# Kernel tuning notes

Measured on AMD Instinct MI355X. Metric: run time of the kernel, lower is better.

Reference implementation:

```python
import jax, jax.numpy as jnp
import numpy as np

B, N_QUBITS, N_LAYERS = 128, 14, 4


def _rx(theta):
    c = jnp.cos(theta / 2).astype(jnp.complex64)
    s = (-1j) * jnp.sin(theta / 2).astype(jnp.complex64)
    return jnp.stack([jnp.stack([c, s], -1), jnp.stack([s, c], -1)], -2)


def _ry(theta):
    c = jnp.cos(theta / 2)
    s = jnp.sin(theta / 2)
    return jnp.stack([jnp.stack([c, -s], -1), jnp.stack([s, c], -1)], -2).astype(jnp.complex64)


def _rz(theta):
    p = jnp.exp((-0.5j) * theta.astype(jnp.complex64))
    q = jnp.exp((0.5j) * theta.astype(jnp.complex64))
    z = jnp.zeros_like(p)
    return jnp.stack([jnp.stack([p, z], -1), jnp.stack([z, q], -1)], -2)


def _apply_1q(state, U, wire):
    # state: (B, 2, 2, ..., 2); U: (2,2) shared or (B,2,2) per-sample
    s = jnp.moveaxis(state, wire + 1, 1)
    if U.ndim == 2:
        s = jnp.einsum('ij,bj...->bi...', U, s)
    else:
        s = jnp.einsum('bij,bj...->bi...', U, s)
    return jnp.moveaxis(s, 1, wire + 1)


def _cnot(state, c, t):
    s = jnp.moveaxis(state, (c + 1, t + 1), (1, 2))  # (B, 2c, 2t, rest)
    s = jnp.concatenate([s[:, :1], s[:, 1:, ::-1]], axis=1)  # flip target where control=1
    return jnp.moveaxis(s, (1, 2), (c + 1, t + 1))


def _layer(state, rx_l, ry_l, rz_l, ent_l, n):
    for i in range(n):
        state = _apply_1q(state, _rx(rx_l[i]), i)
        state = _apply_1q(state, _ry(ry_l[i]), i)
        state = _apply_1q(state, _rz(rz_l[i]), i)
    for i in range(n - 1):
        state = _cnot(state, i, i + 1)
        state = _apply_1q(state, _rz(ent_l[i]), i + 1)
    return state


def _circuit(x, rx_p, ry_p, rz_p, ent_p):
    b, n = x.shape
    n_layers = rx_p.shape[0]
    scaled = jnp.tanh(x) * np.pi  # angle encoding, matches torch.tanh(x)*pi
    state = jnp.zeros((b,) + (2,) * n, jnp.complex64)
    state = state.at[(slice(None),) + (0,) * n].set(1.0)  # |0...0> per sample
    for i in range(n):  # per-sample RY encoding
        state = _apply_1q(state, _ry(scaled[:, i]), i)
    for l in range(n_layers):
        state = _layer(state, rx_p[l], ry_p[l], rz_p[l], ent_p[l], n)
    probs = state.real ** 2 + state.imag ** 2  # (B, 2, ..., 2) real
    outs = []
    for i in range(n):  # <Z_i> = P(bit_i=0) - P(bit_i=1)
        p = jnp.moveaxis(probs, i + 1, 1).reshape(b, 2, -1).sum(-1)
        outs.append(p[:, 0] - p[:, 1])
    return jnp.stack(outs, -1)  # (B, n_qubits)


def setup_inputs() -> dict:
    key = jax.random.key(0)
    k1, k2, k3, k4, k5 = jax.random.split(key, 5)
    return {
        'x': jax.random.normal(k1, (B, N_QUBITS), jnp.float32),
        'params_rx': jax.random.normal(k2, (N_LAYERS, N_QUBITS), jnp.float32),
        'params_ry': jax.random.normal(k3, (N_LAYERS, N_QUBITS), jnp.float32),
        'params_rz': jax.random.normal(k4, (N_LAYERS, N_QUBITS), jnp.float32),
        'params_entangle': jax.random.normal(k5, (N_LAYERS, N_QUBITS - 1), jnp.float32),
    }


def reference(x, params_rx, params_ry, params_rz, params_entangle):
    return _circuit(x, params_rx, params_ry, params_rz, params_entangle)
```

## Files before the change

kernel.cpp:

```cpp
#include <hip/hip_runtime.h>
#include <math.h>

#define NQ 14
#define NL 4
#define NS (1 << NQ)
#define NT 1024
#define APT (NS / NT)

struct c32 { float x, y; };
__device__ __forceinline__ c32 cmul(c32 a, c32 b) { return {a.x*b.x - a.y*b.y, a.x*b.y + a.y*b.x}; }
__device__ __forceinline__ c32 cadd(c32 a, c32 b) { return {a.x + b.x, a.y + b.y}; }

__device__ __forceinline__ c32 phase_mul(float2 p1, float2 p2, float2 f) {
    c32 ph = { p1.x*p2.x - p1.y*p2.y, p1.x*p2.y + p1.y*p2.x };
    return { ph.x*f.x - ph.y*f.y, ph.x*f.y + ph.y*f.x };
}

__device__ __forceinline__ void gate8(c32* v, const float* U, const int s) {
    float4 u0 = *(const float4*)U;
    float4 u1 = *(const float4*)(U + 4);
    c32 a00={u0.x,u0.y}, a01={u0.z,u0.w}, a10={u1.x,u1.y}, a11={u1.z,u1.w};
    #pragma unroll
    for (int k = 0; k < 8; ++k) {
        if (k & s) continue;
        c32 A = v[k], B = v[k | s];
        v[k]     = cadd(cmul(a00, A), cmul(a01, B));
        v[k | s] = cadd(cmul(a10, A), cmul(a11, B));
    }
}

__device__ __forceinline__ void gate4(c32* v, const float* U, const int s) {
    float4 u0 = *(const float4*)U;
    float4 u1 = *(const float4*)(U + 4);
    c32 a00={u0.x,u0.y}, a01={u0.z,u0.w}, a10={u1.x,u1.y}, a11={u1.z,u1.w};
    #pragma unroll
    for (int k = 0; k < 4; ++k) {
        if (k & s) continue;
        c32 A = v[k], B = v[k | s];
        v[k]     = cadd(cmul(a00, A), cmul(a01, B));
        v[k | s] = cadd(cmul(a10, A), cmul(a11, B));
    }
}

__device__ __forceinline__ void gate8sw(c32* v, const float* U, const int s, const int sw) {
    float4 u0 = *(const float4*)U;
    float4 u1 = *(const float4*)(U + 4);
    c32 n00={u0.x,u0.y}, n01={u0.z,u0.w}, n10={u1.x,u1.y}, n11={u1.z,u1.w};
    c32 a00 = sw ? n11 : n00;
    c32 a01 = sw ? n10 : n01;
    c32 a10 = sw ? n01 : n10;
    c32 a11 = sw ? n00 : n11;
    #pragma unroll
    for (int k = 0; k < 8; ++k) {
        if (k & s) continue;
        c32 A = v[k], B = v[k | s];
        v[k]     = cadd(cmul(a00, A), cmul(a01, B));
        v[k | s] = cadd(cmul(a10, A), cmul(a11, B));
    }
}

__global__ __launch_bounds__(NT) __attribute__((amdgpu_waves_per_eu(4, 4)))
void qc_kernel(const float* __restrict__ x,
               const float* __restrict__ prx,
               const float* __restrict__ pry,
               const float* __restrict__ prz,
               const float* __restrict__ pent,
               float* __restrict__ out)
{
    __shared__ float2 st[NS];
    __shared__ float  Um[NL][NQ][8];
    __shared__ float2 tloc[NL][128];
    __shared__ float2 thic[NL][64];
    __shared__ float  encc[NQ], encs[NQ];
    __shared__ float  red[NT/64][NQ];

    const int tid = threadIdx.x;
    const int b   = blockIdx.x;

    if (tid < NL*NQ) {
        int l = tid / NQ, q = tid % NQ;
        float hx = 0.5f*prx[l*NQ+q], hy = 0.5f*pry[l*NQ+q], hz = 0.5f*prz[l*NQ+q];
        float cx = cosf(hx), sx = sinf(hx);
        float cy = cosf(hy), sy = sinf(hy);
        float cz = cosf(hz), sz = sinf(hz);
        c32 m00 = { cy*cx,  sy*sx };
        c32 m01 = {-sy*cx, -cy*sx };
        c32 m10 = { sy*cx, -cy*sx };
        c32 m11 = { cy*cx, -sy*sx };
        c32 e0 = {cz, -sz}, e1 = {cz, sz};
        c32 u00 = cmul(e0, m00), u01 = cmul(e0, m01);
        c32 u10 = cmul(e1, m10), u11 = cmul(e1, m11);
        float* U = Um[l][q];
        U[0]=u00.x; U[1]=u00.y; U[2]=u01.x; U[3]=u01.y;
        U[4]=u10.x; U[5]=u10.y; U[6]=u11.x; U[7]=u11.y;
    } else if (tid >= 64 && tid < 64 + NL*192) {
        int t2 = tid - 64;
        int l = t2 / 192, r = t2 % 192;
        if (r < 128) {
            float a = 0.f;
            for (int p = 0; p < 7; ++p) {
                float th = 0.5f * pent[l*(NQ-1) + (12 - p)];
                a += ((r >> p) & 1) ? th : -th;
            }
            tloc[l][r] = make_float2(cosf(a), sinf(a));
        } else {
            int m = r - 128;
            float a = 0.f;
            for (int p = 0; p < 6; ++p) {
                float th = 0.5f * pent[l*(NQ-1) + (5 - p)];
                a += ((m >> p) & 1) ? th : -th;
            }
            thic[l][m] = make_float2(cosf(a), sinf(a));
        }
    } else if (tid >= 960 && tid < 960 + NQ) {
        int i = tid - 960;
        float th = tanhf(x[b*NQ + i]) * 3.14159265358979323846f;
        encc[i] = cosf(0.5f*th);
        encs[i] = sinf(0.5f*th);
    }
    __syncthreads();

    {
        float prodT = 1.f;
        #pragma unroll
        for (int p = 0; p < 10; ++p)
            prodT *= ((tid >> p) & 1) ? encs[13-p] : encc[13-p];
        #pragma unroll 1
        for (int h = 0; h < 2; ++h) {
            float ah = prodT * (h ? encs[0] : encc[0]);
            c32 v[8];
            #pragma unroll
            for (int m = 0; m < 8; ++m) {
                float a = ah
                        * ((m & 4) ? encs[1] : encc[1])
                        * ((m & 2) ? encs[2] : encc[2])
                        * ((m & 1) ? encs[3] : encc[3]);
                v[m] = { a, 0.f };
            }
            gate8(v, Um[0][1], 4);
            gate8(v, Um[0][2], 2);
            gate8(v, Um[0][3], 1);
            const int yb = (h << 13) | tid;
            #pragma unroll
            for (int m = 0; m < 8; ++m) st[yb + (m << 10)] = make_float2(v[m].x, v[m].y);
        }
    }
    __syncthreads();

    #pragma unroll 1
    for (int l = 0; l < NL; ++l) {
        if (l > 0) {
            #pragma unroll 1
            for (int h = 0; h < 2; ++h) {
                const int yb = (h << 13) | tid;
                c32 v[8];
                #pragma unroll
                for (int m = 0; m < 8; ++m) {
                    int y = yb + (m << 10);
                    int a = y ^ (y >> 1);
                    float2 f = st[a];
                    v[m] = phase_mul(tloc[l-1][y & 127], thic[l-1][(y >> 7) & 63], f);
                }
                gate8(v, Um[l][1], 4);
                gate8(v, Um[l][2], 2);
                gate8(v, Um[l][3], 1);
                __syncthreads();
                #pragma unroll
                for (int m = 0; m < 8; ++m) st[yb + (m << 10)] = make_float2(v[m].x, v[m].y);
            }
            __syncthreads();
        }

        #pragma unroll 1
        for (int m = 0; m < 2; ++m) {
            const int T  = tid + (m << 10);
            const int ib = ((T >> 8) << 10) | (T & 255);
            c32 v[8];
            #pragma unroll
            for (int k = 0; k < 8; ++k) {
                int a = ib + ((k & 4) ? 8192 : 0) + ((k & 2) ? 512 : 0) + ((k & 1) ? 256 : 0);
                float2 f = st[a];
                v[k] = {f.x, f.y};
            }
            gate8(v, Um[l][0], 4);
            gate8(v, Um[l][4], 2);
            gate8(v, Um[l][5], 1);
            #pragma unroll
            for (int k = 0; k < 8; ++k) {
                int a = ib + ((k & 4) ? 8192 : 0) + ((k & 2) ? 512 : 0) + ((k & 1) ? 256 : 0);
                st[a] = make_float2(v[k].x, v[k].y);
            }
        }
        __syncthreads();

        #pragma unroll 1
        for (int m = 0; m < 2; ++m) {
            const int T  = tid + (m << 10);
            const int ib = ((T >> 5) << 8) | (T & 31);
            c32 v[8];
            #pragma unroll
            for (int k = 0; k < 8; ++k) { float2 f = st[ib + (k << 5)]; v[k] = {f.x, f.y}; }
            gate8(v, Um[l][6], 4);
            gate8(v, Um[l][7], 2);
            gate8(v, Um[l][8], 1);
            #pragma unroll
            for (int k = 0; k < 8; ++k) st[ib + (k << 5)] = make_float2(v[k].x, v[k].y);
        }
        __syncthreads();

        #pragma unroll 1
        for (int m = 0; m < 4; ++m) {
            const int T  = tid + (m << 10);
            const int ib = ((T >> 3) << 5) | (T & 7);
            c32 v[4];
            #pragma unroll
            for (int k = 0; k < 4; ++k) { float2 f = st[ib + (k << 3)]; v[k] = {f.x, f.y}; }
            gate4(v, Um[l][9], 2);
            gate4(v, Um[l][10], 1);
            #pragma unroll
            for (int k = 0; k < 4; ++k) st[ib + (k << 3)] = make_float2(v[k].x, v[k].y);
        }
        __syncthreads();

        {
            const int t4   = tid & 15;
            const int base = tid << 4;
            #pragma unroll 1
            for (int m = 0; m < 2; ++m) {
                c32 v[8];
                #pragma unroll
                for (int s = 0; s < 8; ++s) {
                    float2 f = st[base | (((m << 3) | s) ^ t4)];
                    v[s] = {f.x, f.y};
                }
                gate8sw(v, Um[l][11], 4, (t4 >> 2) & 1);
                gate8sw(v, Um[l][12], 2, (t4 >> 1) & 1);
                gate8sw(v, Um[l][13], 1,  t4       & 1);
                #pragma unroll
                for (int s = 0; s < 8; ++s)
                    st[base | (((m << 3) | s) ^ t4)] = make_float2(v[s].x, v[s].y);
            }
        }
        __syncthreads();
    }

    float acc[NQ];
    #pragma unroll
    for (int i = 0; i < NQ; ++i) acc[i] = 0.f;
    #pragma unroll
    for (int j = 0; j < APT; ++j) {
        int y = tid + j*NT;
        int a = y ^ (y >> 1);
        float2 f = st[a];
        c32 r = phase_mul(tloc[NL-1][y & 127], thic[NL-1][(y >> 7) & 63], f);
        float pr = r.x*r.x + r.y*r.y;
        #pragma unroll
        for (int p = 0; p < NQ; ++p)
            acc[NQ-1-p] += ((y >> p) & 1) ? -pr : pr;
    }
    #pragma unroll
    for (int off = 32; off >= 1; off >>= 1) {
        #pragma unroll
        for (int i = 0; i < NQ; ++i)
            acc[i] += __shfl_down(acc[i], off, 64);
    }
    const int wid = tid >> 6, lane = tid & 63;
    if (lane == 0) {
        #pragma unroll
        for (int i = 0; i < NQ; ++i) red[wid][i] = acc[i];
    }
    __syncthreads();
    if (tid < NQ) {
        float s = 0.f;
        #pragma unroll
        for (int w = 0; w < NT/64; ++w) s += red[w][tid];
        out[b*NQ + tid] = s;
    }
}

extern "C" void kernel_launch(void* const* d_in, const int* in_sizes, int n_in,
                              void* d_out, int out_size, void* d_ws, size_t ws_size,
                              hipStream_t stream) {
    (void)d_ws; (void)ws_size; (void)n_in; (void)out_size;
    const float* x    = (const float*)d_in[0];
    const float* prx  = (const float*)d_in[1];
    const float* pry  = (const float*)d_in[2];
    const float* prz  = (const float*)d_in[3];
    const float* pent = (const float*)d_in[4];
    float* out = (float*)d_out;
    const int B = in_sizes[0] / NQ;
    qc_kernel<<<B, NT, 0, stream>>>(x, prx, pry, prz, pent, out);
}
```

Before: 132.6 us.

## Regroup low-qubit gate passes per wavefront to drop block barriers

```diff
diff --git a/kernel.cpp b/kernel.cpp
--- a/kernel.cpp
+++ b/kernel.cpp
@@ -22,19 +22,6 @@
     c32 a00={u0.x,u0.y}, a01={u0.z,u0.w}, a10={u1.x,u1.y}, a11={u1.z,u1.w};
     #pragma unroll
     for (int k = 0; k < 8; ++k) {
-        if (k & s) continue;
-        c32 A = v[k], B = v[k | s];
-        v[k]     = cadd(cmul(a00, A), cmul(a01, B));
-        v[k | s] = cadd(cmul(a10, A), cmul(a11, B));
-    }
-}
-
-__device__ __forceinline__ void gate4(c32* v, const float* U, const int s) {
-    float4 u0 = *(const float4*)U;
-    float4 u1 = *(const float4*)(U + 4);
-    c32 a00={u0.x,u0.y}, a01={u0.z,u0.w}, a10={u1.x,u1.y}, a11={u1.z,u1.w};
-    #pragma unroll
-    for (int k = 0; k < 4; ++k) {
         if (k & s) continue;
         c32 A = v[k], B = v[k | s];
         v[k]     = cadd(cmul(a00, A), cmul(a01, B));
@@ -52,6 +39,23 @@
     c32 a11 = sw ? n00 : n11;
     #pragma unroll
     for (int k = 0; k < 8; ++k) {
+        if (k & s) continue;
+        c32 A = v[k], B = v[k | s];
+        v[k]     = cadd(cmul(a00, A), cmul(a01, B));
+        v[k | s] = cadd(cmul(a10, A), cmul(a11, B));
+    }
+}
+
+__device__ __forceinline__ void gate4sw(c32* v, const float* U, const int s, const int sw) {
+    float4 u0 = *(const float4*)U;
+    float4 u1 = *(const float4*)(U + 4);
+    c32 n00={u0.x,u0.y}, n01={u0.z,u0.w}, n10={u1.x,u1.y}, n11={u1.z,u1.w};
+    c32 a00 = sw ? n11 : n00;
+    c32 a01 = sw ? n10 : n01;
+    c32 a10 = sw ? n01 : n10;
+    c32 a11 = sw ? n00 : n11;
+    #pragma unroll
+    for (int k = 0; k < 4; ++k) {
         if (k & s) continue;
         c32 A = v[k], B = v[k | s];
         v[k]     = cadd(cmul(a00, A), cmul(a01, B));
@@ -193,52 +197,57 @@
         }
         __syncthreads();
 
-        #pragma unroll 1
-        for (int m = 0; m < 2; ++m) {
-            const int T  = tid + (m << 10);
-            const int ib = ((T >> 5) << 8) | (T & 31);
-            c32 v[8];
-            #pragma unroll
-            for (int k = 0; k < 8; ++k) { float2 f = st[ib + (k << 5)]; v[k] = {f.x, f.y}; }
-            gate8(v, Um[l][6], 4);
-            gate8(v, Um[l][7], 2);
-            gate8(v, Um[l][8], 1);
-            #pragma unroll
-            for (int k = 0; k < 8; ++k) st[ib + (k << 5)] = make_float2(v[k].x, v[k].y);
-        }
-        __syncthreads();
-
-        #pragma unroll 1
-        for (int m = 0; m < 4; ++m) {
-            const int T  = tid + (m << 10);
-            const int ib = ((T >> 3) << 5) | (T & 7);
-            c32 v[4];
-            #pragma unroll
-            for (int k = 0; k < 4; ++k) { float2 f = st[ib + (k << 3)]; v[k] = {f.x, f.y}; }
-            gate4(v, Um[l][9], 2);
-            gate4(v, Um[l][10], 1);
-            #pragma unroll
-            for (int k = 0; k < 4; ++k) st[ib + (k << 3)] = make_float2(v[k].x, v[k].y);
-        }
-        __syncthreads();
-
         {
-            const int t4   = tid & 15;
-            const int base = tid << 4;
+            const int lane  = tid & 63;
+            const int wbase = (tid >> 6) << 10;
+
             #pragma unroll 1
             for (int m = 0; m < 2; ++m) {
+                const int t  = (m << 6) | lane;
+                const int ib = wbase | ((t >> 5) << 8) | (t & 31);
                 c32 v[8];
                 #pragma unroll
-                for (int s = 0; s < 8; ++s) {
-                    float2 f = st[base | (((m << 3) | s) ^ t4)];
-                    v[s] = {f.x, f.y};
+                for (int k = 0; k < 8; ++k) { float2 f = st[ib + (k << 5)]; v[k] = {f.x, f.y}; }
+                gate8(v, Um[l][6], 4);
+                gate8(v, Um[l][7], 2);
+                gate8(v, Um[l][8], 1);
+                #pragma unroll
+                for (int k = 0; k < 8; ++k) st[ib + (k << 5)] = make_float2(v[k].x, v[k].y);
+            }
+
+            #pragma unroll 1
+            for (int m = 0; m < 2; ++m) {
+                const int t   = (m << 6) | lane;
+                const int f5  = t >> 2;
+                const int lo2 = t & 3;
+                const int swz = f5 & 3;
+                const int ib  = wbase | (f5 << 5) | lo2;
+                c32 v[8]; int ad[8];
+                #pragma unroll
+                for (int k = 0; k < 8; ++k) {
+                    ad[k] = ib | (((k & 3) ^ swz) << 2) | ((k >> 2) << 4);
+                    float2 f = st[ad[k]];
+                    v[k] = {f.x, f.y};
                 }
-                gate8sw(v, Um[l][11], 4, (t4 >> 2) & 1);
-                gate8sw(v, Um[l][12], 2, (t4 >> 1) & 1);
-                gate8sw(v, Um[l][13], 1,  t4       & 1);
-                #pragma unroll
-                for (int s = 0; s < 8; ++s)
-                    st[base | (((m << 3) | s) ^ t4)] = make_float2(v[s].x, v[s].y);
+                gate8(v, Um[l][9], 4);
+                gate8sw(v, Um[l][10], 2, (swz >> 1) & 1);
+                gate8sw(v, Um[l][11], 1,  swz       & 1);
+                #pragma unroll
+                for (int k = 0; k < 8; ++k) st[ad[k]] = make_float2(v[k].x, v[k].y);
+            }
+
+            #pragma unroll 1
+            for (int m = 0; m < 4; ++m) {
+                const int t   = (m << 6) | lane;
+                const int swz = t & 3;
+                const int ib  = wbase | (t << 2);
+                c32 v[4];
+                #pragma unroll
+                for (int k = 0; k < 4; ++k) { float2 f = st[ib | (k ^ swz)]; v[k] = {f.x, f.y}; }
+                gate4sw(v, Um[l][12], 2, (swz >> 1) & 1);
+                gate4sw(v, Um[l][13], 1,  swz       & 1);
+                #pragma unroll
+                for (int k = 0; k < 4; ++k) st[ib | (k ^ swz)] = make_float2(v[k].x, v[k].y);
             }
         }
         __syncthreads();
```

Result: no change. 135.1 us (+1.9%).

## Add 512-thread kernel with 16 amplitudes per thread and float4 LDS access

Applied to the files above, without the earlier changes.

```diff
diff --git a/kernel.cpp b/kernel.cpp
--- a/kernel.cpp
+++ b/kernel.cpp
@@ -6,6 +6,7 @@
 #define NS (1 << NQ)
 #define NT 1024
 #define APT (NS / NT)
+#define NT5 512
 
 struct c32 { float x, y; };
 __device__ __forceinline__ c32 cmul(c32 a, c32 b) { return {a.x*b.x - a.y*b.y, a.x*b.y + a.y*b.x}; }
@@ -29,12 +30,12 @@
     }
 }
 
-__device__ __forceinline__ void gate4(c32* v, const float* U, const int s) {
+__device__ __forceinline__ void gate16(c32* v, const float* U, const int s) {
     float4 u0 = *(const float4*)U;
     float4 u1 = *(const float4*)(U + 4);
     c32 a00={u0.x,u0.y}, a01={u0.z,u0.w}, a10={u1.x,u1.y}, a11={u1.z,u1.w};
     #pragma unroll
-    for (int k = 0; k < 4; ++k) {
+    for (int k = 0; k < 16; ++k) {
         if (k & s) continue;
         c32 A = v[k], B = v[k | s];
         v[k]     = cadd(cmul(a00, A), cmul(a01, B));
@@ -59,13 +60,264 @@
     }
 }
 
+__device__ __forceinline__ void gate4sw(c32* v, const float* U, const int s, const int sw) {
+    float4 u0 = *(const float4*)U;
+    float4 u1 = *(const float4*)(U + 4);
+    c32 n00={u0.x,u0.y}, n01={u0.z,u0.w}, n10={u1.x,u1.y}, n11={u1.z,u1.w};
+    c32 a00 = sw ? n11 : n00;
+    c32 a01 = sw ? n10 : n01;
+    c32 a10 = sw ? n01 : n10;
+    c32 a11 = sw ? n00 : n11;
+    #pragma unroll
+    for (int k = 0; k < 4; ++k) {
+        if (k & s) continue;
+        c32 A = v[k], B = v[k | s];
+        v[k]     = cadd(cmul(a00, A), cmul(a01, B));
+        v[k | s] = cadd(cmul(a10, A), cmul(a11, B));
+    }
+}
+
+__global__ __launch_bounds__(NT5) __attribute__((amdgpu_waves_per_eu(2, 2)))
+void qc512(const float* __restrict__ x,
+           const float* __restrict__ prx,
+           const float* __restrict__ pry,
+           const float* __restrict__ prz,
+           const float* __restrict__ pent,
+           float* __restrict__ out)
+{
+    __shared__ __align__(16) float2 st[NS];
+    __shared__ float  Um[NL][NQ][8];
+    __shared__ float2 tloc[NL][128];
+    __shared__ float2 thic[NL][64];
+    __shared__ float  encc[NQ], encs[NQ];
+    __shared__ float  red[NT5/64][NQ];
+
+    const int tid = threadIdx.x;
+    const int b   = blockIdx.x;
+    float4* st4 = reinterpret_cast<float4*>(st);
+
+    if (tid < NL*NQ) {
+        int l = tid / NQ, q = tid % NQ;
+        float hx = 0.5f*prx[l*NQ+q], hy = 0.5f*pry[l*NQ+q], hz = 0.5f*prz[l*NQ+q];
+        float cx = cosf(hx), sx = sinf(hx);
+        float cy = cosf(hy), sy = sinf(hy);
+        float cz = cosf(hz), sz = sinf(hz);
+        c32 m00 = { cy*cx,  sy*sx };
+        c32 m01 = {-sy*cx, -cy*sx };
+        c32 m10 = { sy*cx, -cy*sx };
+        c32 m11 = { cy*cx, -sy*sx };
+        c32 e0 = {cz, -sz}, e1 = {cz, sz};
+        c32 u00 = cmul(e0, m00), u01 = cmul(e0, m01);
+        c32 u10 = cmul(e1, m10), u11 = cmul(e1, m11);
+        float* U = Um[l][q];
+        U[0]=u00.x; U[1]=u00.y; U[2]=u01.x; U[3]=u01.y;
+        U[4]=u10.x; U[5]=u10.y; U[6]=u11.x; U[7]=u11.y;
+    }
+    for (int e = tid; e < NL*192; e += NT5) {
+        int l = e / 192, r = e % 192;
+        if (r < 128) {
+            float a = 0.f;
+            for (int p = 0; p < 7; ++p) {
+                float th = 0.5f * pent[l*(NQ-1) + (12 - p)];
+                a += ((r >> p) & 1) ? th : -th;
+            }
+            tloc[l][r] = make_float2(cosf(a), sinf(a));
+        } else {
+            int m = r - 128;
+            float a = 0.f;
+            for (int p = 0; p < 6; ++p) {
+                float th = 0.5f * pent[l*(NQ-1) + (5 - p)];
+                a += ((m >> p) & 1) ? th : -th;
+            }
+            thic[l][m] = make_float2(cosf(a), sinf(a));
+        }
+    }
+    if (tid >= 480 && tid < 480 + NQ) {
+        int i = tid - 480;
+        float th = tanhf(x[b*NQ + i]) * 3.14159265358979323846f;
+        encc[i] = cosf(0.5f*th);
+        encs[i] = sinf(0.5f*th);
+    }
+    __syncthreads();
+
+    {
+        float prodT = 1.f;
+        #pragma unroll
+        for (int bb = 0; bb < 9; ++bb)
+            prodT *= ((tid >> bb) & 1) ? encs[12-bb] : encc[12-bb];
+        #pragma unroll 1
+        for (int h = 0; h < 2; ++h) {
+            float ah = prodT * (h ? encs[0] : encc[0]);
+            c32 v[16];
+            #pragma unroll
+            for (int k = 0; k < 8; ++k) {
+                float kf = ((k & 4) ? encs[1] : encc[1])
+                         * ((k & 2) ? encs[2] : encc[2])
+                         * ((k & 1) ? encs[3] : encc[3]);
+                v[(k<<1)]   = { ah * kf * encc[13], 0.f };
+                v[(k<<1)|1] = { ah * kf * encs[13], 0.f };
+            }
+            gate16(v, Um[0][1], 8);
+            gate16(v, Um[0][2], 4);
+            gate16(v, Um[0][3], 2);
+            #pragma unroll
+            for (int k = 0; k < 8; ++k)
+                st4[(h<<12) | (k<<9) | tid] =
+                    make_float4(v[(k<<1)].x, v[(k<<1)].y, v[(k<<1)|1].x, v[(k<<1)|1].y);
+        }
+    }
+    __syncthreads();
+
+    #pragma unroll 1
+    for (int l = 0; l < NL; ++l) {
+        if (l > 0) {
+            const int swp = tid & 1;
+            #pragma unroll 1
+            for (int h = 0; h < 2; ++h) {
+                c32 v[16];
+                #pragma unroll
+                for (int k = 0; k < 8; ++k) {
+                    int y0 = (h<<13) | (k<<10) | (tid<<1);
+                    int x0 = y0 ^ (y0 >> 1);
+                    float4 q = st4[x0 >> 1];
+                    float2 s0 = swp ? make_float2(q.z, q.w) : make_float2(q.x, q.y);
+                    float2 s1 = swp ? make_float2(q.x, q.y) : make_float2(q.z, q.w);
+                    int y1 = y0 | 1;
+                    v[(k<<1)]   = phase_mul(tloc[l-1][y0 & 127], thic[l-1][(y0 >> 7) & 63], s0);
+                    v[(k<<1)|1] = phase_mul(tloc[l-1][y1 & 127], thic[l-1][(y1 >> 7) & 63], s1);
+                }
+                gate16(v, Um[l][1], 8);
+                gate16(v, Um[l][2], 4);
+                gate16(v, Um[l][3], 2);
+                __syncthreads();
+                #pragma unroll
+                for (int k = 0; k < 8; ++k)
+                    st4[(h<<12) | (k<<9) | tid] =
+                        make_float4(v[(k<<1)].x, v[(k<<1)].y, v[(k<<1)|1].x, v[(k<<1)|1].y);
+            }
+            __syncthreads();
+        }
+
+        #pragma unroll 1
+        for (int m = 0; m < 2; ++m) {
+            const int u = (m << 9) | tid;
+            const int fb = ((u >> 7) << 9) | (u & 127);
+            c32 v[16];
+            #pragma unroll
+            for (int k = 0; k < 8; ++k) {
+                int fidx = fb | ((k & 4) ? 4096 : 0) | ((k & 2) ? 256 : 0) | ((k & 1) ? 128 : 0);
+                float4 q = st4[fidx];
+                v[(k<<1)]   = { q.x, q.y };
+                v[(k<<1)|1] = { q.z, q.w };
+            }
+            gate16(v, Um[l][0], 8);
+            gate16(v, Um[l][4], 4);
+            gate16(v, Um[l][5], 2);
+            #pragma unroll
+            for (int k = 0; k < 8; ++k) {
+                int fidx = fb | ((k & 4) ? 4096 : 0) | ((k & 2) ? 256 : 0) | ((k & 1) ? 128 : 0);
+                st4[fidx] = make_float4(v[(k<<1)].x, v[(k<<1)].y, v[(k<<1)|1].x, v[(k<<1)|1].y);
+            }
+        }
+        __syncthreads();
+
+        #pragma unroll 1
+        for (int m = 0; m < 2; ++m) {
+            const int u = (m << 9) | tid;
+            const int fb = ((u >> 4) << 7) | (u & 15);
+            c32 v[16];
+            #pragma unroll
+            for (int k = 0; k < 8; ++k) {
+                float4 q = st4[fb | (k << 4)];
+                v[(k<<1)]   = { q.x, q.y };
+                v[(k<<1)|1] = { q.z, q.w };
+            }
+            gate16(v, Um[l][6], 8);
+            gate16(v, Um[l][7], 4);
+            gate16(v, Um[l][8], 2);
+            #pragma unroll
+            for (int k = 0; k < 8; ++k)
+                st4[fb | (k << 4)] = make_float4(v[(k<<1)].x, v[(k<<1)].y, v[(k<<1)|1].x, v[(k<<1)|1].y);
+        }
+        __syncthreads();
+
+        {
+            const int x5   = tid & 31;
+            const int base = tid << 5;
+            #pragma unroll 1
+            for (int g = 0; g < 8; ++g) {
+                c32 v[4];
+                #pragma unroll
+                for (int k = 0; k < 4; ++k) {
+                    float2 f = st[base | (((k << 3) | g) ^ x5)];
+                    v[k] = {f.x, f.y};
+                }
+                gate4sw(v, Um[l][9],  2, (x5 >> 4) & 1);
+                gate4sw(v, Um[l][10], 1, (x5 >> 3) & 1);
+                #pragma unroll
+                for (int k = 0; k < 4; ++k)
+                    st[base | (((k << 3) | g) ^ x5)] = make_float2(v[k].x, v[k].y);
+            }
+            #pragma unroll 1
+            for (int g2 = 0; g2 < 4; ++g2) {
+                c32 v[8];
+                #pragma unroll
+                for (int s = 0; s < 8; ++s) {
+                    float2 f = st[base | (((g2 << 3) | s) ^ x5)];
+                    v[s] = {f.x, f.y};
+                }
+                gate8sw(v, Um[l][11], 4, (x5 >> 2) & 1);
+                gate8sw(v, Um[l][12], 2, (x5 >> 1) & 1);
+                gate8sw(v, Um[l][13], 1,  x5       & 1);
+                #pragma unroll
+                for (int s = 0; s < 8; ++s)
+                    st[base | (((g2 << 3) | s) ^ x5)] = make_float2(v[s].x, v[s].y);
+            }
+        }
+        __syncthreads();
+    }
+
+    float acc[NQ];
+    #pragma unroll
+    for (int i = 0; i < NQ; ++i) acc[i] = 0.f;
+    #pragma unroll
+    for (int j = 0; j < 32; ++j) {
+        int y = tid + (j << 9);
+        int a = y ^ (y >> 1);
+        float2 f = st[a];
+        c32 r = phase_mul(tloc[NL-1][y & 127], thic[NL-1][(y >> 7) & 63], f);
+        float pr = r.x*r.x + r.y*r.y;
+        #pragma unroll
+        for (int p = 0; p < NQ; ++p)
+            acc[NQ-1-p] += ((y >> p) & 1) ? -pr : pr;
+    }
+    #pragma unroll
+    for (int off = 32; off >= 1; off >>= 1) {
+        #pragma unroll
+        for (int i = 0; i < NQ; ++i)
+            acc[i] += __shfl_down(acc[i], off, 64);
+    }
+    const int wid = tid >> 6, lane = tid & 63;
+    if (lane == 0) {
+        #pragma unroll
+        for (int i = 0; i < NQ; ++i) red[wid][i] = acc[i];
+    }
+    __syncthreads();
+    if (tid < NQ) {
+        float s = 0.f;
+        #pragma unroll
+        for (int w = 0; w < NT5/64; ++w) s += red[w][tid];
+        out[b*NQ + tid] = s;
+    }
+}
+
 __global__ __launch_bounds__(NT) __attribute__((amdgpu_waves_per_eu(4, 4)))
-void qc_kernel(const float* __restrict__ x,
-               const float* __restrict__ prx,
-               const float* __restrict__ pry,
-               const float* __restrict__ prz,
-               const float* __restrict__ pent,
-               float* __restrict__ out)
+void qc1024(const float* __restrict__ x,
+            const float* __restrict__ prx,
+            const float* __restrict__ pry,
+            const float* __restrict__ prz,
+            const float* __restrict__ pent,
+            float* __restrict__ out)
 {
     __shared__ float2 st[NS];
     __shared__ float  Um[NL][NQ][8];
@@ -215,8 +467,8 @@
             c32 v[4];
             #pragma unroll
             for (int k = 0; k < 4; ++k) { float2 f = st[ib + (k << 3)]; v[k] = {f.x, f.y}; }
-            gate4(v, Um[l][9], 2);
-            gate4(v, Um[l][10], 1);
+            gate4sw(v, Um[l][9], 2, 0);
+            gate4sw(v, Um[l][10], 1, 0);
             #pragma unroll
             for (int k = 0; k < 4; ++k) st[ib + (k << 3)] = make_float2(v[k].x, v[k].y);
         }
@@ -289,5 +541,15 @@
     const float* pent = (const float*)d_in[4];
     float* out = (float*)d_out;
     const int B = in_sizes[0] / NQ;
-    qc_kernel<<<B, NT, 0, stream>>>(x, prx, pry, prz, pent, out);
-}
+
+    static int use512 = -1;
+    if (use512 < 0) {
+        hipFuncAttributes attr;
+        hipError_t err = hipFuncGetAttributes(&attr, (const void*)qc512);
+        use512 = (err == hipSuccess && attr.localSizeBytes == 0) ? 1 : 0;
+    }
+    if (use512)
+        qc512<<<B, NT5, 0, stream>>>(x, prx, pry, prz, pent, out);
+    else
+        qc1024<<<B, NT, 0, stream>>>(x, prx, pry, prz, pent, out);
+}
```

Result: no change. 135.1 us (+1.9%).
